# Performance work log

Hardware: AMD Instinct MI355X
Metric: run time of the kernel (lower is better)

The kernel has to match this reference:

```python
import jax, jax.numpy as jnp
import numpy as np

LEAK = 0.01
EPS = 1e-5


def _gcn(x, W, b, src, dst, n):
    # GCNConv: add self-loops, symmetric D^-1/2 (A+I) D^-1/2 normalization
    h = x @ W
    loop = jnp.arange(n)
    s = jnp.concatenate([src, loop])
    d = jnp.concatenate([dst, loop])
    deg = jax.ops.segment_sum(jnp.ones(s.shape[0], h.dtype), d, num_segments=n)
    dinv = jnp.where(deg > 0, jax.lax.rsqrt(deg), 0.0)
    norm = dinv[s] * dinv[d]
    out = jax.ops.segment_sum(h[s] * norm[:, None], d, num_segments=n)
    return out + b


def _sage(x, Wl, bl, Wr, src, dst, n):
    # SAGEConv (mean aggr): lin_l(mean_neigh) + lin_r(x); bias on lin_l
    cnt = jax.ops.segment_sum(jnp.ones(src.shape[0], x.dtype), dst, num_segments=n)
    agg = jax.ops.segment_sum(x[src], dst, num_segments=n) / jnp.maximum(cnt, 1.0)[:, None]
    return agg @ Wl + bl + x @ Wr


def _bn(x, g, b):
    # BatchNorm over node dim, batch statistics (training forward), biased var
    m = x.mean(0)
    v = jnp.mean((x - m) ** 2, axis=0)
    return (x - m) * jax.lax.rsqrt(v + EPS) * g + b


def _lrelu(x):
    return jnp.where(x >= 0, x, LEAK * x)


def setup_inputs() -> dict:
    key = jax.random.key(0)
    ks = jax.random.split(key, 20)
    N, E, F_IN, H, G, L = 50000, 800000, 128, 128, 1000, 1000
    h2, h4, OUT = H // 2, H // 4, 32
    x = jax.random.normal(ks[0], (N, F_IN), dtype=jnp.float32)
    edge_index = jax.random.randint(ks[1], (2, E), 0, N)
    batch = jnp.sort(jax.random.randint(ks[2], (N,), 0, G))
    link_indices = jax.random.randint(ks[3], (2, L), 0, G)
    s = 0.05
    return {
        "x": x, "edge_index": edge_index, "batch": batch,
        "link_indices": link_indices, "num_graphs": G,
        "W1": jax.random.normal(ks[4], (F_IN, H), jnp.float32) * s,
        "b1": jnp.zeros((H,), jnp.float32),
        "g1": jnp.ones((H,), jnp.float32), "be1": jnp.zeros((H,), jnp.float32),
        "Wl2": jax.random.normal(ks[5], (H, h2), jnp.float32) * s,
        "bl2": jnp.zeros((h2,), jnp.float32),
        "Wr2": jax.random.normal(ks[6], (H, h2), jnp.float32) * s,
        "g2": jnp.ones((h2,), jnp.float32), "be2": jnp.zeros((h2,), jnp.float32),
        "W3": jax.random.normal(ks[7], (h2, h4), jnp.float32) * s,
        "b3": jnp.zeros((h4,), jnp.float32),
        "g3": jnp.ones((h4,), jnp.float32), "be3": jnp.zeros((h4,), jnp.float32),
        "W4": jax.random.normal(ks[8], (h4, OUT), jnp.float32) * s,
        "b4": jnp.zeros((OUT,), jnp.float32),
    }


def reference(x, edge_index, batch, link_indices, num_graphs,
              W1, b1, g1, be1, Wl2, bl2, Wr2, g2, be2,
              W3, b3, g3, be3, W4, b4):
    n = x.shape[0]
    src, dst = edge_index[0], edge_index[1]
    h = _lrelu(_bn(_gcn(x, W1, b1, src, dst, n), g1, be1))        # dropout = identity (eval)
    h = _lrelu(_bn(_sage(h, Wl2, bl2, Wr2, src, dst, n), g2, be2))
    h = _lrelu(_bn(_gcn(h, W3, b3, src, dst, n), g3, be3))
    h = _gcn(h, W4, b4, src, dst, n)
    g = jax.ops.segment_sum(h, batch, num_segments=num_graphs)     # global_add_pool
    src_emb = g[link_indices[0]]
    tgt_emb = g[link_indices[1]]
    return jax.nn.sigmoid(jnp.sum(src_emb * tgt_emb, axis=1))
```

## Files before the change

kernel.cpp:

```cpp
#include <hip/hip_runtime.h>
#include <math.h>

#define LEAK 0.01f
#define BNEPS 1e-5f
#define NCH 256
#define NGMAX 1024

typedef __attribute__((ext_vector_type(8))) short bf16x8;
typedef __attribute__((ext_vector_type(4))) float f32x4;

__device__ inline unsigned bfpack(float a, float b) {
  unsigned ua = __float_as_uint(a);
  unsigned ub = __float_as_uint(b);
  unsigned ra = (ua + 0x7fffu + ((ua >> 16) & 1u)) >> 16;
  unsigned rb = (ub + 0x7fffu + ((ub >> 16) & 1u)) & 0xffff0000u;
  return ra | rb;
}
__device__ inline unsigned short bfround(float a) {
  unsigned ua = __float_as_uint(a);
  return (unsigned short)((ua + 0x7fffu + ((ua >> 16) & 1u)) >> 16);
}
__device__ inline float2 bfunpack(unsigned u) {
  float2 r;
  r.x = __uint_as_float(u << 16);
  r.y = __uint_as_float(u & 0xffff0000u);
  return r;
}

__global__ __launch_bounds__(256) void k_hist(const int* __restrict__ dst,
                                              int* __restrict__ H, int E, int NBK) {
  __shared__ int h[256];
  h[threadIdx.x] = 0;
  __syncthreads();
  int chunk = (E + NCH - 1) / NCH;
  int lo = blockIdx.x * chunk, hi = min(lo + chunk, E);
  for (int e = lo + threadIdx.x; e < hi; e += 256)
    atomicAdd(&h[dst[e] >> 8], 1);
  __syncthreads();
  if (threadIdx.x < NBK) H[threadIdx.x * NCH + blockIdx.x] = h[threadIdx.x];
}

__global__ __launch_bounds__(256) void k_gscan1(const int* __restrict__ in,
                                                int* __restrict__ bsum, int m) {
  int i = blockIdx.x * 256 + threadIdx.x;
  int v = (i < m) ? in[i] : 0;
#pragma unroll
  for (int s = 1; s < 64; s <<= 1) v += __shfl_xor(v, s, 64);
  __shared__ int ws[4];
  if ((threadIdx.x & 63) == 0) ws[threadIdx.x >> 6] = v;
  __syncthreads();
  if (threadIdx.x == 0) bsum[blockIdx.x] = ws[0] + ws[1] + ws[2] + ws[3];
}
__global__ __launch_bounds__(256) void k_gscan2(int* __restrict__ bsum, int NB) {
  __shared__ int lds[256];
  int t = threadIdx.x;
  int v = (t < NB) ? bsum[t] : 0;
  lds[t] = v;
  __syncthreads();
  for (int ofs = 1; ofs < 256; ofs <<= 1) {
    int u = (t >= ofs) ? lds[t - ofs] : 0;
    __syncthreads();
    lds[t] += u;
    __syncthreads();
  }
  if (t < NB) bsum[t] = lds[t] - v;
}
__global__ __launch_bounds__(256) void k_gscan3(const int* __restrict__ in,
                                                const int* __restrict__ boff,
                                                int* __restrict__ out, int m) {
  __shared__ int lds[256];
  int t = threadIdx.x;
  int i = blockIdx.x * 256 + t;
  int v = (i < m) ? in[i] : 0;
  lds[t] = v;
  __syncthreads();
  for (int ofs = 1; ofs < 256; ofs <<= 1) {
    int u = (t >= ofs) ? lds[t - ofs] : 0;
    __syncthreads();
    lds[t] += u;
    __syncthreads();
  }
  if (i < m) out[i] = boff[blockIdx.x] + lds[t] - v;
}

__global__ __launch_bounds__(256) void k_scatter_bkt(
    const int* __restrict__ src, const int* __restrict__ dst,
    const int* __restrict__ O, int* __restrict__ ebuf, int E, int NBK) {
  __shared__ int cur[256];
  if (threadIdx.x < NBK) cur[threadIdx.x] = O[threadIdx.x * NCH + blockIdx.x];
  __syncthreads();
  int chunk = (E + NCH - 1) / NCH;
  int lo = blockIdx.x * chunk, hi = min(lo + chunk, E);
  for (int e = lo + threadIdx.x; e < hi; e += 256) {
    int d = dst[e];
    int pos = atomicAdd(&cur[d >> 8], 1);
    ebuf[pos] = src[e] | ((d & 255) << 24);
  }
}

__global__ __launch_bounds__(256) void k_fill2(
    const int* __restrict__ ebuf, const int* __restrict__ O,
    int* __restrict__ eidx, int* __restrict__ rowptr,
    float* __restrict__ dinv, float* __restrict__ invcnt,
    int E, int n, int NBK) {
  __shared__ int hist[256];
  __shared__ int sc[256];
  __shared__ int cur[256];
  const int b = blockIdx.x;
  const int t = threadIdx.x;
  const int lo = O[b * NCH];
  const int hi = (b + 1 < NBK) ? O[(b + 1) * NCH] : E;
  hist[t] = 0;
  __syncthreads();
  for (int e = lo + t; e < hi; e += 256)
    atomicAdd(&hist[(ebuf[e] >> 24) & 255], 1);
  __syncthreads();
  int v = hist[t];
  sc[t] = v;
  __syncthreads();
  for (int ofs = 1; ofs < 256; ofs <<= 1) {
    int u = (t >= ofs) ? sc[t - ofs] : 0;
    __syncthreads();
    sc[t] += u;
    __syncthreads();
  }
  int excl = sc[t] - v;
  cur[t] = lo + excl;
  int node = b * 256 + t;
  if (node < n) {
    rowptr[node] = lo + excl;
    float d = (float)v;
    dinv[node]   = rsqrtf(d + 1.0f);
    invcnt[node] = 1.0f / fmaxf(d, 1.0f);
  }
  if (node == n || (b == NBK - 1 && t == 255)) rowptr[n] = E;
  __syncthreads();
  for (int e = lo + t; e < hi; e += 256) {
    int p = ebuf[e];
    int pos = atomicAdd(&cur[(p >> 24) & 255], 1);
    eidx[pos] = p & 0xFFFFFF;
  }
}

template<int F, bool GCN, bool OUTBF, bool ADD>
__global__ __launch_bounds__(256) void k_gather(
    const unsigned short* __restrict__ Hs, const float* __restrict__ scale,
    const int* __restrict__ rowptr, const int* __restrict__ eidx,
    const float* __restrict__ bias, const float* __restrict__ addf,
    float* __restrict__ outf, unsigned short* __restrict__ outb, int n) {
  constexpr int COLS = F / 8;
  constexpr int EPI  = 64 / COLS;
  const int v = blockIdx.x * 4 + (threadIdx.x >> 6);
  if (v >= n) return;
  const int lane = threadIdx.x & 63;
  const int col  = lane % COLS;
  const int eo   = lane / COLS;

  const int lo = rowptr[v], hi = rowptr[v + 1];
  float a[8] = {0.f,0.f,0.f,0.f,0.f,0.f,0.f,0.f};
  int myE = (lo + lane < hi) ? eidx[lo + lane] : 0;
  for (int base = lo; base < hi; base += 64) {
    int cnt = min(hi - base, 64);
    int nxt = (base + 64 + lane < hi) ? eidx[base + 64 + lane] : 0;
#pragma unroll 4
    for (int t = eo; t < cnt; t += EPI) {
      int s = __shfl(myE, t, 64);
      uint4 hv = *(const uint4*)&Hs[(long long)s * F + col * 8];
      float2 p0 = bfunpack(hv.x), p1 = bfunpack(hv.y);
      float2 p2 = bfunpack(hv.z), p3 = bfunpack(hv.w);
      a[0]+=p0.x; a[1]+=p0.y; a[2]+=p1.x; a[3]+=p1.y;
      a[4]+=p2.x; a[5]+=p2.y; a[6]+=p3.x; a[7]+=p3.y;
    }
    myE = nxt;
  }
#pragma unroll
  for (int m = COLS; m < 64; m <<= 1) {
#pragma unroll
    for (int j = 0; j < 8; j++) a[j] += __shfl_xor(a[j], m, 64);
  }
  if (eo == 0) {
    float sv = scale[v];
    float o[8];
    if constexpr (GCN) {
      uint4 hv = *(const uint4*)&Hs[(long long)v * F + col * 8];
      float2 p0 = bfunpack(hv.x), p1 = bfunpack(hv.y);
      float2 p2 = bfunpack(hv.z), p3 = bfunpack(hv.w);
      float h[8] = {p0.x,p0.y,p1.x,p1.y,p2.x,p2.y,p3.x,p3.y};
#pragma unroll
      for (int j = 0; j < 8; j++) o[j] = bias[col * 8 + j] + sv * (a[j] + h[j]);
    } else if constexpr (ADD) {
      const float4 t0 = *(const float4*)&addf[(long long)v * F + col * 8];
      const float4 t1 = *(const float4*)&addf[(long long)v * F + col * 8 + 4];
      o[0]=fmaf(sv,a[0],t0.x); o[1]=fmaf(sv,a[1],t0.y);
      o[2]=fmaf(sv,a[2],t0.z); o[3]=fmaf(sv,a[3],t0.w);
      o[4]=fmaf(sv,a[4],t1.x); o[5]=fmaf(sv,a[5],t1.y);
      o[6]=fmaf(sv,a[6],t1.z); o[7]=fmaf(sv,a[7],t1.w);
    } else {
#pragma unroll
      for (int j = 0; j < 8; j++) o[j] = sv * a[j];
    }
    if constexpr (OUTBF) {
      uint4 u;
      u.x = bfpack(o[0], o[1]); u.y = bfpack(o[2], o[3]);
      u.z = bfpack(o[4], o[5]); u.w = bfpack(o[6], o[7]);
      *(uint4*)&outb[(long long)v * F + col * 8] = u;
    } else {
      float4 o0 = {o[0],o[1],o[2],o[3]}, o1 = {o[4],o[5],o[6],o[7]};
      *(float4*)&outf[(long long)v * F + col * 8]     = o0;
      *(float4*)&outf[(long long)v * F + col * 8 + 4] = o1;
    }
  }
}

template<int K, int F, bool XBF, bool BNIN>
__global__ __launch_bounds__(256) void k_gemm_mfma(
    const void* __restrict__ Xv, const float* __restrict__ W,
    const float* __restrict__ bnstats, const float* __restrict__ prescale,
    unsigned short* __restrict__ Yb, int n) {
  constexpr int SP  = K + 8;
  constexpr int NCT = F / 16;
  __shared__ unsigned short sX[64 * SP];
  __shared__ unsigned short sWT[F * SP];
  __shared__ float sbn[BNIN ? 2 * K : 1];

  const int row0 = blockIdx.x * 64;
  if constexpr (BNIN) {
    for (int i = threadIdx.x; i < 2 * K; i += 256) sbn[i] = bnstats[i];
    __syncthreads();
  }
  for (int i = threadIdx.x; i < (K / 2) * F; i += 256) {
    int nn = i % F;
    int kk = (i / F) * 2;
    float w0 = W[(long long)kk * F + nn];
    float w1 = W[(long long)(kk + 1) * F + nn];
    *(unsigned*)&sWT[nn * SP + kk] = bfpack(w0, w1);
  }
  for (int i = threadIdx.x; i < 64 * (K / 8); i += 256) {
    int r = i / (K / 8), k8 = (i % (K / 8)) * 8;
    int gr = row0 + r;
    uint4 u = {0, 0, 0, 0};
    if (gr < n) {
      if constexpr (XBF) {
        const unsigned short* X = (const unsigned short*)Xv;
        uint4 raw = *(const uint4*)&X[(long long)gr * K + k8];
        if constexpr (BNIN) {
          float2 p0 = bfunpack(raw.x), p1 = bfunpack(raw.y);
          float2 p2 = bfunpack(raw.z), p3 = bfunpack(raw.w);
          float y[8] = {p0.x,p0.y,p1.x,p1.y,p2.x,p2.y,p3.x,p3.y};
#pragma unroll
          for (int j = 0; j < 8; j++) {
            float t = fmaf(y[j], sbn[k8 + j], sbn[K + k8 + j]);
            y[j] = (t >= 0.f) ? t : LEAK * t;
          }
          u.x = bfpack(y[0], y[1]); u.y = bfpack(y[2], y[3]);
          u.z = bfpack(y[4], y[5]); u.w = bfpack(y[6], y[7]);
        } else {
          u = raw;
        }
      } else {
        const float* X = (const float*)Xv;
        float4 xa = *(const float4*)&X[(long long)gr * K + k8];
        float4 xb = *(const float4*)&X[(long long)gr * K + k8 + 4];
        u.x = bfpack(xa.x, xa.y); u.y = bfpack(xa.z, xa.w);
        u.z = bfpack(xb.x, xb.y); u.w = bfpack(xb.z, xb.w);
      }
    }
    *(uint4*)&sX[r * SP + k8] = u;
  }
  __syncthreads();

  const int wv   = threadIdx.x >> 6;
  const int lane = threadIdx.x & 63;
  const int l16  = lane & 15;
  const int quad = lane >> 4;
  f32x4 acc[NCT];
#pragma unroll
  for (int c = 0; c < NCT; c++) acc[c] = (f32x4){0.f, 0.f, 0.f, 0.f};

#pragma unroll
  for (int k0 = 0; k0 < K; k0 += 32) {
    bf16x8 af = *(const bf16x8*)&sX[(wv * 16 + l16) * SP + k0 + quad * 8];
#pragma unroll
    for (int c = 0; c < NCT; c++) {
      bf16x8 bfr = *(const bf16x8*)&sWT[(c * 16 + l16) * SP + k0 + quad * 8];
      acc[c] = __builtin_amdgcn_mfma_f32_16x16x32_bf16(af, bfr, acc[c], 0, 0, 0);
    }
  }

  const int rbase = row0 + wv * 16 + quad * 4;
  float ps[4];
#pragma unroll
  for (int rg = 0; rg < 4; rg++) {
    int gr = rbase + rg;
    ps[rg] = (prescale && gr < n) ? prescale[gr] : 1.0f;
  }
#pragma unroll
  for (int c = 0; c < NCT; c++) {
    int col = c * 16 + l16;
#pragma unroll
    for (int rg = 0; rg < 4; rg++) {
      int gr = rbase + rg;
      if (gr < n) Yb[(long long)gr * F + col] = bfround(acc[c][rg] * ps[rg]);
    }
  }
}

__global__ __launch_bounds__(256) void k_gemm_sage_mfma(
    const unsigned short* __restrict__ X, const float* __restrict__ Wl,
    const float* __restrict__ Wr, const float* __restrict__ bl,
    const float* __restrict__ bnstats,
    unsigned short* __restrict__ t1, float* __restrict__ t2, int n) {
  constexpr int K = 128, F = 64, SP = K + 8, NCT = F / 16;
  __shared__ unsigned short sX[64 * SP];
  __shared__ unsigned short sWlT[F * SP];
  __shared__ unsigned short sWrT[F * SP];
  __shared__ float sbn[2 * K];

  for (int i = threadIdx.x; i < 2 * K; i += 256) sbn[i] = bnstats[i];
  __syncthreads();
  const int row0 = blockIdx.x * 64;
  for (int i = threadIdx.x; i < (K / 2) * F; i += 256) {
    int nn = i % F;
    int kk = (i / F) * 2;
    *(unsigned*)&sWlT[nn * SP + kk] =
        bfpack(Wl[(long long)kk * F + nn], Wl[(long long)(kk + 1) * F + nn]);
    *(unsigned*)&sWrT[nn * SP + kk] =
        bfpack(Wr[(long long)kk * F + nn], Wr[(long long)(kk + 1) * F + nn]);
  }
  for (int i = threadIdx.x; i < 64 * (K / 8); i += 256) {
    int r = i / (K / 8), k8 = (i % (K / 8)) * 8;
    int gr = row0 + r;
    uint4 u = {0, 0, 0, 0};
    if (gr < n) {
      uint4 raw = *(const uint4*)&X[(long long)gr * K + k8];
      float2 p0 = bfunpack(raw.x), p1 = bfunpack(raw.y);
      float2 p2 = bfunpack(raw.z), p3 = bfunpack(raw.w);
      float y[8] = {p0.x,p0.y,p1.x,p1.y,p2.x,p2.y,p3.x,p3.y};
#pragma unroll
      for (int j = 0; j < 8; j++) {
        float t = fmaf(y[j], sbn[k8 + j], sbn[K + k8 + j]);
        y[j] = (t >= 0.f) ? t : LEAK * t;
      }
      u.x = bfpack(y[0], y[1]); u.y = bfpack(y[2], y[3]);
      u.z = bfpack(y[4], y[5]); u.w = bfpack(y[6], y[7]);
    }
    *(uint4*)&sX[r * SP + k8] = u;
  }
  __syncthreads();

  const int wv   = threadIdx.x >> 6;
  const int lane = threadIdx.x & 63;
  const int l16  = lane & 15;
  const int quad = lane >> 4;
  f32x4 a1[NCT], a2[NCT];
#pragma unroll
  for (int c = 0; c < NCT; c++) {
    a1[c] = (f32x4){0.f, 0.f, 0.f, 0.f};
    a2[c] = (f32x4){0.f, 0.f, 0.f, 0.f};
  }
#pragma unroll
  for (int k0 = 0; k0 < K; k0 += 32) {
    bf16x8 af = *(const bf16x8*)&sX[(wv * 16 + l16) * SP + k0 + quad * 8];
#pragma unroll
    for (int c = 0; c < NCT; c++) {
      bf16x8 bl8 = *(const bf16x8*)&sWlT[(c * 16 + l16) * SP + k0 + quad * 8];
      bf16x8 br8 = *(const bf16x8*)&sWrT[(c * 16 + l16) * SP + k0 + quad * 8];
      a1[c] = __builtin_amdgcn_mfma_f32_16x16x32_bf16(af, bl8, a1[c], 0, 0, 0);
      a2[c] = __builtin_amdgcn_mfma_f32_16x16x32_bf16(af, br8, a2[c], 0, 0, 0);
    }
  }
  const int rbase = row0 + wv * 16 + quad * 4;
#pragma unroll
  for (int c = 0; c < NCT; c++) {
    int col = c * 16 + l16;
    float blv = bl[col];
#pragma unroll
    for (int rg = 0; rg < 4; rg++) {
      int gr = rbase + rg;
      if (gr < n) {
        t1[(long long)gr * F + col] = bfround(a1[c][rg]);
        t2[(long long)gr * F + col] = a2[c][rg] + blv;
      }
    }
  }
}

template<int F>
__global__ __launch_bounds__(256) void k_bn_stats(const unsigned short* __restrict__ Y,
                                                  float* __restrict__ partials, int n) {
  constexpr int FP  = F / 2;
  constexpr int RPB = 256 / FP;
  const int f2 = threadIdx.x % FP;
  const int r0 = threadIdx.x / FP;
  const unsigned* Yu = (const unsigned*)Y;
  float s1a = 0.f, s2a = 0.f, s1b = 0.f, s2b = 0.f;
  for (long long r = (long long)blockIdx.x * RPB + r0; r < n; r += 256LL * RPB) {
    float2 p = bfunpack(Yu[r * FP + f2]);
    s1a += p.x; s2a += p.x * p.x;
    s1b += p.y; s2b += p.y * p.y;
  }
  __shared__ float l1a[256], l2a[256], l1b[256], l2b[256];
  l1a[threadIdx.x] = s1a; l2a[threadIdx.x] = s2a;
  l1b[threadIdx.x] = s1b; l2b[threadIdx.x] = s2b;
  __syncthreads();
  if (r0 == 0) {
#pragma unroll
    for (int i = 1; i < RPB; i++) {
      s1a += l1a[i * FP + f2]; s2a += l2a[i * FP + f2];
      s1b += l1b[i * FP + f2]; s2b += l2b[i * FP + f2];
    }
    float* p = &partials[blockIdx.x * 2 * F];
    p[2 * f2]         = s1a;
    p[2 * f2 + 1]     = s1b;
    p[F + 2 * f2]     = s2a;
    p[F + 2 * f2 + 1] = s2b;
  }
}

__global__ void k_bn_finalize(const float* __restrict__ partials, float* __restrict__ stats,
                              const float* __restrict__ g, const float* __restrict__ be,
                              int F, float invN) {
  int f = threadIdx.x;
  if (f >= F) return;
  float s1 = 0.f, s2 = 0.f;
  for (int b = 0; b < 256; b++) {
    s1 += partials[b * 2 * F + f];
    s2 += partials[b * 2 * F + F + f];
  }
  float m   = s1 * invN;
  float var = s2 * invN - m * m;
  float sc  = g[f] * rsqrtf(var + BNEPS);
  stats[f]     = sc;
  stats[F + f] = be[f] - m * sc;
}

__global__ __launch_bounds__(256) void k_pool2(const float* __restrict__ a4,
                                               const int* __restrict__ batch,
                                               float* __restrict__ gpool, int n) {
  int g = blockIdx.x * 4 + (threadIdx.x >> 6);
  if (g >= NGMAX) return;
  int lane = threadIdx.x & 63;
  int s = 0, e = n;
  while (s < e) { int m = (s + e) >> 1; if (batch[m] < g) s = m + 1; else e = m; }
  int s2 = s, e2 = n;
  while (s2 < e2) { int m = (s2 + e2) >> 1; if (batch[m] < g + 1) s2 = m + 1; else e2 = m; }
  int f = lane & 31, ro = lane >> 5;
  float acc = 0.f;
  for (int r = s + ro; r < s2; r += 2) acc += a4[(long long)r * 32 + f];
  acc += __shfl_xor(acc, 32, 64);
  if (lane < 32) gpool[(long long)g * 32 + f] = acc;
}

__global__ void k_link(const float* __restrict__ g, const int* __restrict__ li0,
                       const int* __restrict__ li1, float* __restrict__ out, int L) {
  int i = blockIdx.x * blockDim.x + threadIdx.x;
  if (i >= L) return;
  const float* a = g + (long long)li0[i] * 32;
  const float* b = g + (long long)li1[i] * 32;
  float s = 0.f;
#pragma unroll
  for (int f = 0; f < 32; f++) s = fmaf(a[f], b[f], s);
  out[i] = 1.0f / (1.0f + expf(-s));
}

extern "C" void kernel_launch(void* const* d_in, const int* in_sizes, int n_in,
                              void* d_out, int out_size, void* d_ws, size_t ws_size,
                              hipStream_t stream) {
  const float* x   = (const float*)d_in[0];
  const int* ei    = (const int*)d_in[1];
  const int* batch = (const int*)d_in[2];
  const int* li    = (const int*)d_in[3];
  const float* W1  = (const float*)d_in[5];
  const float* b1  = (const float*)d_in[6];
  const float* g1  = (const float*)d_in[7];
  const float* be1 = (const float*)d_in[8];
  const float* Wl2 = (const float*)d_in[9];
  const float* bl2 = (const float*)d_in[10];
  const float* Wr2 = (const float*)d_in[11];
  const float* g2  = (const float*)d_in[12];
  const float* be2 = (const float*)d_in[13];
  const float* W3  = (const float*)d_in[14];
  const float* b3  = (const float*)d_in[15];
  const float* g3  = (const float*)d_in[16];
  const float* be3 = (const float*)d_in[17];
  const float* W4  = (const float*)d_in[18];
  const float* b4  = (const float*)d_in[19];

  const int n = in_sizes[0] / 128;
  const int E = in_sizes[1] / 2;
  const int L = in_sizes[3] / 2;
  const int* src = ei;
  const int* dst = ei + E;
  const int* li0 = li;
  const int* li1 = li + L;
  const int NBK = (n + 255) / 256;

  char* base = (char*)d_ws;
  size_t off = 0;
  auto alloc = [&](size_t bytes) -> void* {
    void* p = (void*)(base + off);
    off = (off + bytes + 255) & ~(size_t)255;
    return p;
  };
  int*   H      = (int*)alloc((size_t)NBK * NCH * 4);
  int*   O      = (int*)alloc((size_t)NBK * NCH * 4);
  int*   hsum   = (int*)alloc(1024 * 4);
  int*   ebuf   = (int*)alloc((size_t)E * 4);
  int*   eidx   = (int*)alloc((size_t)E * 4);
  int*   rowptr = (int*)alloc((size_t)(n + 1) * 4);
  float* dinv   = (float*)alloc((size_t)n * 4);
  float* invcnt = (float*)alloc((size_t)n * 4);
  float* stats1 = (float*)alloc(256 * 4);
  float* stats2 = (float*)alloc(128 * 4);
  float* stats3 = (float*)alloc(64 * 4);
  float* partials = (float*)alloc((size_t)256 * 256 * 4);
  float* gpool  = (float*)alloc((size_t)NGMAX * 32 * 4);
  unsigned short* h1b  = (unsigned short*)alloc((size_t)n * 128 * 2);
  unsigned short* a1b  = (unsigned short*)alloc((size_t)n * 128 * 2);
  unsigned short* t1b  = (unsigned short*)alloc((size_t)n * 64 * 2);
  float*          t2f  = (float*)alloc((size_t)n * 64 * 4);
  unsigned short* h2b  = (unsigned short*)alloc((size_t)n * 64 * 2);
  unsigned short* h3gb = (unsigned short*)alloc((size_t)n * 32 * 2);
  unsigned short* a3b  = (unsigned short*)alloc((size_t)n * 32 * 2);
  unsigned short* h4b  = (unsigned short*)alloc((size_t)n * 32 * 2);
  float*          a4f  = (float*)alloc((size_t)n * 32 * 4);
  (void)ws_size; (void)n_in; (void)out_size;

  const int BT = 256;
  auto cdiv = [](long long a, long long b) { return (int)((a + b - 1) / b); };
  const int GB  = cdiv(n, 4);
  const int GM  = cdiv(n, 64);
  const int MH  = NBK * NCH;
  const int NBH = cdiv(MH, 256);

  k_hist<<<NCH, 256, 0, stream>>>(dst, H, E, NBK);
  k_gscan1<<<NBH, 256, 0, stream>>>(H, hsum, MH);
  k_gscan2<<<1, 256, 0, stream>>>(hsum, NBH);
  k_gscan3<<<NBH, 256, 0, stream>>>(H, hsum, O, MH);
  k_scatter_bkt<<<NCH, 256, 0, stream>>>(src, dst, O, ebuf, E, NBK);
  k_fill2<<<NBK, 256, 0, stream>>>(ebuf, O, eidx, rowptr, dinv, invcnt, E, n, NBK);

  k_gemm_mfma<128,128,false,false><<<GM, 256, 0, stream>>>(
      x, W1, nullptr, dinv, h1b, n);
  k_gather<128,true,true,false><<<GB, 256, 0, stream>>>(
      h1b, dinv, rowptr, eidx, b1, nullptr, nullptr, a1b, n);
  k_bn_stats<128><<<256, 256, 0, stream>>>(a1b, partials, n);
  k_bn_finalize<<<1, 128, 0, stream>>>(partials, stats1, g1, be1, 128, 1.0f / n);

  k_gemm_sage_mfma<<<GM, 256, 0, stream>>>(a1b, Wl2, Wr2, bl2, stats1, t1b, t2f, n);
  k_gather<64,false,true,true><<<GB, 256, 0, stream>>>(
      t1b, invcnt, rowptr, eidx, nullptr, t2f, nullptr, h2b, n);
  k_bn_stats<64><<<256, 256, 0, stream>>>(h2b, partials, n);
  k_bn_finalize<<<1, 64, 0, stream>>>(partials, stats2, g2, be2, 64, 1.0f / n);

  k_gemm_mfma<64,32,true,true><<<GM, 256, 0, stream>>>(
      h2b, W3, stats2, dinv, h3gb, n);
  k_gather<32,true,true,false><<<GB, 256, 0, stream>>>(
      h3gb, dinv, rowptr, eidx, b3, nullptr, nullptr, a3b, n);
  k_bn_stats<32><<<256, 256, 0, stream>>>(a3b, partials, n);
  k_bn_finalize<<<1, 32, 0, stream>>>(partials, stats3, g3, be3, 32, 1.0f / n);

  k_gemm_mfma<32,32,true,true><<<GM, 256, 0, stream>>>(
      a3b, W4, stats3, dinv, h4b, n);
  k_gather<32,true,false,false><<<GB, 256, 0, stream>>>(
      h4b, dinv, rowptr, eidx, b4, nullptr, a4f, nullptr, n);

  k_pool2<<<NGMAX / 4, 256, 0, stream>>>(a4f, batch, gpool, n);
  k_link<<<cdiv(L, BT), BT, 0, stream>>>(gpool, li0, li1, (float*)d_out, L);
}
```

Before: 381.0 us.

## Gather first GCN layer from FP8 copy of features, keep bf16 self term

The first GEMM now also writes an FP8 copy of the normalized features. A new dedicated gather kernel reads neighbor rows from that copy, halving the bytes per edge. The self-loop term still comes from the bf16 copy, and accumulation stays in fp32. NCH is also reduced from 256 to 64, which changes the histogram and scatter chunking. The risk is reduced accuracy from FP8 quantization of the aggregated messages, plus an extra byte-wise strided store in the GEMM epilogue.

```diff
diff --git a/kernel.cpp b/kernel.cpp
--- a/kernel.cpp
+++ b/kernel.cpp
@@ -3,11 +3,12 @@
 
 #define LEAK 0.01f
 #define BNEPS 1e-5f
-#define NCH 256
+#define NCH 64
 #define NGMAX 1024
 
 typedef __attribute__((ext_vector_type(8))) short bf16x8;
 typedef __attribute__((ext_vector_type(4))) float f32x4;
+typedef __attribute__((ext_vector_type(2))) float f32x2;
 
 __device__ inline unsigned bfpack(float a, float b) {
   unsigned ua = __float_as_uint(a);
@@ -25,6 +26,10 @@
   r.x = __uint_as_float(u << 16);
   r.y = __uint_as_float(u & 0xffff0000u);
   return r;
+}
+__device__ inline unsigned char f32_to_fp8(float v) {
+  int p = __builtin_amdgcn_cvt_pk_fp8_f32(v, v, 0, false);
+  return (unsigned char)(p & 0xff);
 }
 
 __global__ __launch_bounds__(256) void k_hist(const int* __restrict__ dst,
@@ -212,11 +217,63 @@
   }
 }
 
-template<int K, int F, bool XBF, bool BNIN>
+__global__ __launch_bounds__(256) void k_gather_gcn_fp8(
+    const unsigned char* __restrict__ Hf8, const unsigned short* __restrict__ Hbf,
+    const float* __restrict__ scale,
+    const int* __restrict__ rowptr, const int* __restrict__ eidx,
+    const float* __restrict__ bias, unsigned short* __restrict__ outb, int n) {
+  constexpr int F = 128, COLS = 16, EPI = 4;
+  const int v = blockIdx.x * 4 + (threadIdx.x >> 6);
+  if (v >= n) return;
+  const int lane = threadIdx.x & 63;
+  const int col  = lane % COLS;
+  const int eo   = lane / COLS;
+
+  const int lo = rowptr[v], hi = rowptr[v + 1];
+  float a[8] = {0.f,0.f,0.f,0.f,0.f,0.f,0.f,0.f};
+  int myE = (lo + lane < hi) ? eidx[lo + lane] : 0;
+  for (int base = lo; base < hi; base += 64) {
+    int cnt = min(hi - base, 64);
+    int nxt = (base + 64 + lane < hi) ? eidx[base + 64 + lane] : 0;
+#pragma unroll 4
+    for (int t = eo; t < cnt; t += EPI) {
+      int s = __shfl(myE, t, 64);
+      uint2 q = *(const uint2*)&Hf8[(long long)s * F + col * 8];
+      f32x2 p0 = __builtin_amdgcn_cvt_pk_f32_fp8(q.x, false);
+      f32x2 p1 = __builtin_amdgcn_cvt_pk_f32_fp8(q.x, true);
+      f32x2 p2 = __builtin_amdgcn_cvt_pk_f32_fp8(q.y, false);
+      f32x2 p3 = __builtin_amdgcn_cvt_pk_f32_fp8(q.y, true);
+      a[0]+=p0[0]; a[1]+=p0[1]; a[2]+=p1[0]; a[3]+=p1[1];
+      a[4]+=p2[0]; a[5]+=p2[1]; a[6]+=p3[0]; a[7]+=p3[1];
+    }
+    myE = nxt;
+  }
+#pragma unroll
+  for (int m = COLS; m < 64; m <<= 1) {
+#pragma unroll
+    for (int j = 0; j < 8; j++) a[j] += __shfl_xor(a[j], m, 64);
+  }
+  if (eo == 0) {
+    float sv = scale[v];
+    uint4 hv = *(const uint4*)&Hbf[(long long)v * F + col * 8];
+    float2 p0 = bfunpack(hv.x), p1 = bfunpack(hv.y);
+    float2 p2 = bfunpack(hv.z), p3 = bfunpack(hv.w);
+    float h[8] = {p0.x,p0.y,p1.x,p1.y,p2.x,p2.y,p3.x,p3.y};
+    float o[8];
+#pragma unroll
+    for (int j = 0; j < 8; j++) o[j] = bias[col * 8 + j] + sv * (a[j] + h[j]);
+    uint4 u;
+    u.x = bfpack(o[0], o[1]); u.y = bfpack(o[2], o[3]);
+    u.z = bfpack(o[4], o[5]); u.w = bfpack(o[6], o[7]);
+    *(uint4*)&outb[(long long)v * F + col * 8] = u;
+  }
+}
+
+template<int K, int F, bool XBF, bool BNIN, bool F8OUT>
 __global__ __launch_bounds__(256) void k_gemm_mfma(
     const void* __restrict__ Xv, const float* __restrict__ W,
     const float* __restrict__ bnstats, const float* __restrict__ prescale,
-    unsigned short* __restrict__ Yb, int n) {
+    unsigned short* __restrict__ Yb, unsigned char* __restrict__ Yf8, int n) {
   constexpr int SP  = K + 8;
   constexpr int NCT = F / 16;
   __shared__ unsigned short sX[64 * SP];
@@ -300,7 +357,11 @@
 #pragma unroll
     for (int rg = 0; rg < 4; rg++) {
       int gr = rbase + rg;
-      if (gr < n) Yb[(long long)gr * F + col] = bfround(acc[c][rg] * ps[rg]);
+      if (gr < n) {
+        float val = acc[c][rg] * ps[rg];
+        Yb[(long long)gr * F + col] = bfround(val);
+        if constexpr (F8OUT) Yf8[(long long)gr * F + col] = f32_to_fp8(val);
+      }
     }
   }
 }
@@ -516,6 +577,7 @@
   float* partials = (float*)alloc((size_t)256 * 256 * 4);
   float* gpool  = (float*)alloc((size_t)NGMAX * 32 * 4);
   unsigned short* h1b  = (unsigned short*)alloc((size_t)n * 128 * 2);
+  unsigned char*  h1f8 = (unsigned char*)alloc((size_t)n * 128);
   unsigned short* a1b  = (unsigned short*)alloc((size_t)n * 128 * 2);
   unsigned short* t1b  = (unsigned short*)alloc((size_t)n * 64 * 2);
   float*          t2f  = (float*)alloc((size_t)n * 64 * 4);
@@ -540,10 +602,10 @@
   k_scatter_bkt<<<NCH, 256, 0, stream>>>(src, dst, O, ebuf, E, NBK);
   k_fill2<<<NBK, 256, 0, stream>>>(ebuf, O, eidx, rowptr, dinv, invcnt, E, n, NBK);
 
-  k_gemm_mfma<128,128,false,false><<<GM, 256, 0, stream>>>(
-      x, W1, nullptr, dinv, h1b, n);
-  k_gather<128,true,true,false><<<GB, 256, 0, stream>>>(
-      h1b, dinv, rowptr, eidx, b1, nullptr, nullptr, a1b, n);
+  k_gemm_mfma<128,128,false,false,true><<<GM, 256, 0, stream>>>(
+      x, W1, nullptr, dinv, h1b, h1f8, n);
+  k_gather_gcn_fp8<<<GB, 256, 0, stream>>>(
+      h1f8, h1b, dinv, rowptr, eidx, b1, a1b, n);
   k_bn_stats<128><<<256, 256, 0, stream>>>(a1b, partials, n);
   k_bn_finalize<<<1, 128, 0, stream>>>(partials, stats1, g1, be1, 128, 1.0f / n);
 
@@ -553,15 +615,15 @@
   k_bn_stats<64><<<256, 256, 0, stream>>>(h2b, partials, n);
   k_bn_finalize<<<1, 64, 0, stream>>>(partials, stats2, g2, be2, 64, 1.0f / n);
 
-  k_gemm_mfma<64,32,true,true><<<GM, 256, 0, stream>>>(
-      h2b, W3, stats2, dinv, h3gb, n);
+  k_gemm_mfma<64,32,true,true,false><<<GM, 256, 0, stream>>>(
+      h2b, W3, stats2, dinv, h3gb, nullptr, n);
   k_gather<32,true,true,false><<<GB, 256, 0, stream>>>(
       h3gb, dinv, rowptr, eidx, b3, nullptr, nullptr, a3b, n);
   k_bn_stats<32><<<256, 256, 0, stream>>>(a3b, partials, n);
   k_bn_finalize<<<1, 32, 0, stream>>>(partials, stats3, g3, be3, 32, 1.0f / n);
 
-  k_gemm_mfma<32,32,true,true><<<GM, 256, 0, stream>>>(
-      a3b, W4, stats3, dinv, h4b, n);
+  k_gemm_mfma<32,32,true,true,false><<<GM, 256, 0, stream>>>(
+      a3b, W4, stats3, dinv, h4b, nullptr, n);
   k_gather<32,true,false,false><<<GB, 256, 0, stream>>>(
       h4b, dinv, rowptr, eidx, b4, nullptr, a4f, nullptr, n);
 
```

Result: slower. 403.6 us (+5.9%).
